# Kernel optimization log

Hardware: AMD Instinct MI355X
Metric: run time of the kernel (lower is better)

## Reference

```python
import jax, jax.numpy as jnp
import numpy as np

VAR0, VAR1 = 0.1, 0.2
THRESHOLD = 0.35
NEGPOS_RATIO = 7
LOW_GT_THRESH = 0.2  # match() filters GT whose best prior IoU < 0.2


def setup_inputs() -> dict:
    key = jax.random.key(0)
    ks = jax.random.split(key, 8)
    B, P, G = 16, 43008, 128
    loc_data = jax.random.normal(ks[0], (B, P, 4), jnp.float32)
    conf_data = jax.random.normal(ks[1], (B, P, 2), jnp.float32)
    landm_data = jax.random.normal(ks[2], (B, P, 10), jnp.float32)
    # priors in cxcywh form, positive sizes
    pc = jax.random.uniform(ks[3], (P, 2), jnp.float32)
    pwh = jax.random.uniform(ks[4], (P, 2), jnp.float32, minval=0.02, maxval=0.32)
    priors = jnp.concatenate([pc, pwh], axis=1)
    # targets: valid xyxy boxes + 10 landmark coords + label (face=1)
    ctr = jax.random.uniform(ks[5], (B, G, 2), jnp.float32, minval=0.2, maxval=0.8)
    wh = jax.random.uniform(ks[6], (B, G, 2), jnp.float32, minval=0.05, maxval=0.3)
    boxes = jnp.concatenate([ctr - wh / 2, ctr + wh / 2], axis=-1)
    landms = jax.random.uniform(ks[7], (B, G, 10), jnp.float32)
    labels = jnp.ones((B, G, 1), jnp.float32)
    targets = jnp.concatenate([boxes, landms, labels], axis=-1)
    return {"loc_data": loc_data, "conf_data": conf_data, "landm_data": landm_data,
            "priors": priors, "targets": targets}


def point_form(priors):
    return jnp.concatenate([priors[:, :2] - priors[:, 2:] / 2,
                            priors[:, :2] + priors[:, 2:] / 2], axis=1)


def jaccard(a, b):  # a: [G,4] xyxy, b: [P,4] xyxy -> [G,P]
    lt = jnp.maximum(a[:, None, :2], b[None, :, :2])
    rb = jnp.minimum(a[:, None, 2:], b[None, :, 2:])
    wh = jnp.clip(rb - lt, 0.0)
    inter = wh[..., 0] * wh[..., 1]
    area_a = (a[:, 2] - a[:, 0]) * (a[:, 3] - a[:, 1])
    area_b = (b[:, 2] - b[:, 0]) * (b[:, 3] - b[:, 1])
    return inter / (area_a[:, None] + area_b[None, :] - inter)


def encode(matched, priors):  # matched xyxy [P,4], priors cxcywh [P,4]
    g_cxcy = (matched[:, :2] + matched[:, 2:]) / 2 - priors[:, :2]
    g_cxcy = g_cxcy / (VAR0 * priors[:, 2:])
    g_wh = jnp.log((matched[:, 2:] - matched[:, :2]) / priors[:, 2:]) / VAR1
    return jnp.concatenate([g_cxcy, g_wh], axis=1)


def encode_landm(matched, priors):  # matched [P,10], priors [P,4]
    m = matched.reshape(-1, 5, 2)
    g = (m - priors[:, None, :2]) / (VAR0 * priors[:, None, 2:])
    return g.reshape(-1, 10)


def match_one(truths, labels, landms, priors):
    G = truths.shape[0]
    overlaps = jaccard(truths, point_form(priors))  # [G, P]
    best_prior_overlap = overlaps.max(axis=1)       # [G]
    best_prior_idx = overlaps.argmax(axis=1)        # [G]
    valid = best_prior_overlap >= LOW_GT_THRESH
    any_valid = jnp.any(valid)
    best_truth_overlap = overlaps.max(axis=0)       # [P]
    best_truth_idx = overlaps.argmax(axis=0)        # [P]
    # index_fill_(0, best_prior_idx_filter, 2): ensure each valid GT keeps its best prior
    fill_val = jnp.where(valid, 2.0, best_truth_overlap[best_prior_idx])
    best_truth_overlap = best_truth_overlap.at[best_prior_idx].set(fill_val)
    # best_truth_idx[best_prior_idx[j]] = j for all j
    best_truth_idx = best_truth_idx.at[best_prior_idx].set(jnp.arange(G))
    matches = truths[best_truth_idx]                       # [P,4]
    conf = labels[best_truth_idx].astype(jnp.int32)        # [P]
    conf = jnp.where(best_truth_overlap < THRESHOLD, 0, conf)
    conf = jnp.where(any_valid, conf, 0)  # no valid GT -> all background
    loc = encode(matches, priors)
    landm = encode_landm(landms[best_truth_idx], priors)
    return loc, conf, landm


def smooth_l1(x):
    ax = jnp.abs(x)
    return jnp.where(ax < 1.0, 0.5 * ax * ax, ax - 0.5)


def reference(loc_data, conf_data, landm_data, priors, targets):
    truths = targets[..., :4]
    landms = targets[..., 4:14]
    labels = targets[..., 14]
    loc_t, conf_t, landm_t = jax.vmap(
        lambda t, l, lm: match_one(t, l, lm, priors))(truths, labels, landms)

    # landmark loss over positives
    pos1 = conf_t > 0
    N1 = jnp.maximum(pos1.sum().astype(jnp.float32), 1.0)
    loss_landm = jnp.sum(smooth_l1(landm_data - landm_t) * pos1[..., None])

    # localization loss over positives
    pos = conf_t != 0
    num_pos = pos.sum(axis=1, keepdims=True)  # [B,1]
    loss_l = jnp.sum(smooth_l1(loc_data - loc_t) * pos[..., None])

    # hard negative mining on per-prior CE loss
    lse = jax.scipy.special.logsumexp(conf_data, axis=-1)  # [B,P]
    gathered = jnp.take_along_axis(conf_data, conf_t[..., None], axis=-1)[..., 0]
    ce_all = lse - gathered                                # [B,P] per-prior CE
    mine = jnp.where(pos, 0.0, ce_all)
    loss_idx = jnp.argsort(-mine, axis=1)
    idx_rank = jnp.argsort(loss_idx, axis=1)
    num_neg = jnp.clip(NEGPOS_RATIO * num_pos, None, pos.shape[1] - 1)
    neg = idx_rank < num_neg
    sel = pos | neg
    loss_c = jnp.sum(jnp.where(sel, ce_all, 0.0))

    N = jnp.maximum(num_pos.sum().astype(jnp.float32), 1.0)
    return loss_l / N, loss_c / N, loss_landm / N1
```

## Files before the change

kernel.cpp:

```cpp
#include <hip/hip_runtime.h>
#include <stdint.h>


#define GC 8
#define PPI 3

__device__ __forceinline__ float sl1(float x) {
  float a = fabsf(x);
  return a < 1.f ? 0.5f * a * a : a - 0.5f;
}

__device__ __forceinline__ double dwave(double v) {
#pragma unroll
  for (int o = 32; o; o >>= 1) v += __shfl_down(v, o);
  return v;
}

__global__ __launch_bounds__(256) void k_match(
    const float* __restrict__ priors, const float* __restrict__ targets,
    float* __restrict__ bto, int* __restrict__ bti,
    unsigned long long* __restrict__ bp, int P, int G, int NIOU, int PT3,
    int NGC, int PC) {
  int tid = threadIdx.x;
  __shared__ float4 sgt[128];
  __shared__ float sga[128];
  __shared__ unsigned long long sred[GC * 256];

  if ((int)blockIdx.x < NIOU) {
    int b = blockIdx.x / PT3, tile = blockIdx.x % PT3;
    int base = tile * (256 * PPI);
    for (int g = tid; g < G; g += 256) {
      const float* t = targets + ((size_t)b * G + g) * 15;
      float x1 = t[0], y1 = t[1], x2 = t[2], y2 = t[3];
      sgt[g] = make_float4(x1, y1, x2, y2);
      sga[g] = (x2 - x1) * (y2 - y1);
    }
    __syncthreads();

    float px1[PPI], py1[PPI], px2[PPI], py2[PPI], pa[PPI];
    float bi[PPI], sb[PPI];
    int bidx[PPI];
#pragma unroll
    for (int k = 0; k < PPI; ++k) {
      int p = base + tid + k * 256;
      int pl = p < P ? p : P - 1;
      float4 pr = ((const float4*)priors)[pl];
      px1[k] = pr.x - pr.z * 0.5f; py1[k] = pr.y - pr.w * 0.5f;
      px2[k] = pr.x + pr.z * 0.5f; py2[k] = pr.y + pr.w * 0.5f;
      pa[k] = pr.z * pr.w;
      bi[k] = 0.f; sb[k] = 1.f; bidx[k] = 0;
    }

    for (int g = 0; g < G; g += 2) {
      float4 T0 = sgt[g];
      float4 T1 = sgt[g + 1];
      float A0 = sga[g];
      float A1 = sga[g + 1];
#pragma unroll
      for (int k = 0; k < PPI; ++k) {
        {
          float iw = fminf(T0.z, px2[k]) - fmaxf(T0.x, px1[k]);
          float ih = fminf(T0.w, py2[k]) - fmaxf(T0.y, py1[k]);
          float inter = fmaxf(iw, 0.f) * fmaxf(ih, 0.f);
          float S = A0 + pa[k];
          if (inter * sb[k] > bi[k] * S) { bi[k] = inter; sb[k] = S; bidx[k] = g; }
        }
        {
          float iw = fminf(T1.z, px2[k]) - fmaxf(T1.x, px1[k]);
          float ih = fminf(T1.w, py2[k]) - fmaxf(T1.y, py1[k]);
          float inter = fmaxf(iw, 0.f) * fmaxf(ih, 0.f);
          float S = A1 + pa[k];
          if (inter * sb[k] > bi[k] * S) { bi[k] = inter; sb[k] = S; bidx[k] = g + 1; }
        }
      }
    }
#pragma unroll
    for (int k = 0; k < PPI; ++k) {
      int p = base + tid + k * 256;
      if (p < P) {
        bto[(size_t)b * P + p] = bi[k] / (sb[k] - bi[k]);
        bti[(size_t)b * P + p] = bidx[k];
      }
    }
  } else {
    int bc = blockIdx.x - NIOU;
    int pc = bc % PC;
    int gcb = (bc / PC) % NGC;
    int b = bc / (PC * NGC);
    int g0 = gcb * GC;

    if (tid < GC) {
      int g = g0 + tid;
      float4 v = make_float4(0.f, 0.f, 0.f, 0.f);
      if (g < G) {
        const float* t = targets + ((size_t)b * G + g) * 15;
        v = make_float4(t[0], t[1], t[2], t[3]);
      }
      sgt[tid] = v;
    }
    __syncthreads();

    float gx1[GC], gy1[GC], gx2[GC], gy2[GC], ga[GC];
#pragma unroll
    for (int j = 0; j < GC; ++j) {
      float4 T = sgt[j];
      gx1[j] = T.x; gy1[j] = T.y; gx2[j] = T.z; gy2[j] = T.w;
      ga[j] = (T.z - T.x) * (T.w - T.y);
    }

    int chunk = (P + PC - 1) / PC;
    int ps = pc * chunk;
    int pe = ps + chunk; if (pe > P) pe = P;
    int count = pe - ps;

    float bi[GC], sb[GC];
    unsigned bpp[GC];
#pragma unroll
    for (int j = 0; j < GC; ++j) { bi[j] = 0.f; sb[j] = 1.f; bpp[j] = (unsigned)(ps + tid); }

    for (int i = tid; i < count; i += 512) {
      int p0 = ps + i;
      int i1 = i + 256;
      int p1 = (i1 < count) ? ps + i1 : p0;
      float4 q0 = ((const float4*)priors)[p0];
      float4 q1 = ((const float4*)priors)[p1];
      float ax1 = q0.x - q0.z * 0.5f, ay1 = q0.y - q0.w * 0.5f;
      float ax2 = q0.x + q0.z * 0.5f, ay2 = q0.y + q0.w * 0.5f;
      float aa = q0.z * q0.w;
      float bx1 = q1.x - q1.z * 0.5f, by1 = q1.y - q1.w * 0.5f;
      float bx2 = q1.x + q1.z * 0.5f, by2 = q1.y + q1.w * 0.5f;
      float ba = q1.z * q1.w;
#pragma unroll
      for (int j = 0; j < GC; ++j) {
        {
          float iw = fminf(gx2[j], ax2) - fmaxf(gx1[j], ax1);
          float ih = fminf(gy2[j], ay2) - fmaxf(gy1[j], ay1);
          float inter = fmaxf(iw, 0.f) * fmaxf(ih, 0.f);
          float S = ga[j] + aa;
          if (inter * sb[j] > bi[j] * S) { bi[j] = inter; sb[j] = S; bpp[j] = (unsigned)p0; }
        }
        {
          float iw = fminf(gx2[j], bx2) - fmaxf(gx1[j], bx1);
          float ih = fminf(gy2[j], by2) - fmaxf(gy1[j], by1);
          float inter = fmaxf(iw, 0.f) * fmaxf(ih, 0.f);
          float S = ga[j] + ba;
          if (inter * sb[j] > bi[j] * S) { bi[j] = inter; sb[j] = S; bpp[j] = (unsigned)p1; }
        }
      }
    }

#pragma unroll
    for (int j = 0; j < GC; ++j) {
      float iou = bi[j] / (sb[j] - bi[j]);
      unsigned long long pk =
          ((unsigned long long)__float_as_uint(iou) << 32) | (unsigned)(~bpp[j]);
      sred[j * 256 + tid] = pk;
    }
    __syncthreads();
    {
      int j = tid >> 5, s = tid & 31;
      unsigned long long m = sred[j * 256 + s];
#pragma unroll
      for (int t = 1; t < 8; ++t) {
        unsigned long long v = sred[j * 256 + s + t * 32];
        if (v > m) m = v;
      }
      __syncthreads();
      sred[j * 256 + s] = m;
    }
    __syncthreads();
    if (tid < GC) {
      unsigned long long m = sred[tid * 256];
      for (int s = 1; s < 32; ++s) {
        unsigned long long v = sred[tid * 256 + s];
        if (v > m) m = v;
      }
      int g = g0 + tid;
      if (g < G) atomicMax(&bp[(size_t)b * G + g], m);
    }
  }
}

__global__ void k_scatter(const unsigned long long* __restrict__ bp,
                          float* __restrict__ bto, int* __restrict__ bti,
                          int* __restrict__ anyv, int P, int G) {
  int b = blockIdx.x, g = threadIdx.x;
  __shared__ unsigned spp[128];
  __shared__ int s_any;
  if (g == 0) s_any = 0;
  __syncthreads();
  unsigned long long m = bp[(size_t)b * G + g];
  unsigned pp = ~(unsigned)m;
  float val = __uint_as_float((unsigned)(m >> 32));
  bool ok = (m != 0ULL);
  float oldv = 0.f;
  if (ok) oldv = bto[(size_t)b * P + pp];
  spp[g] = ok ? pp : 0xFFFFFFFFu;
  if (ok && val >= 0.2f) s_any = 1;
  __syncthreads();
  bool win = ok;
  for (int g2 = g + 1; g2 < G; ++g2)
    if (spp[g2] == pp) win = false;
  if (win) {
    bto[(size_t)b * P + pp] = (val >= 0.2f) ? 2.0f : oldv;
    bti[(size_t)b * P + pp] = g;
  }
  __syncthreads();
  if (g == 0) anyv[b] = s_any;
}

__global__ __launch_bounds__(256) void k_main(
    const float* __restrict__ loc, const float* __restrict__ conf,
    const float* __restrict__ lm, const float* __restrict__ priors,
    const float* __restrict__ targets, const float* __restrict__ bto,
    const int* __restrict__ bti, const int* __restrict__ anyv,
    float* __restrict__ mine, unsigned* __restrict__ h1,
    double* __restrict__ pll, double* __restrict__ pllm,
    double* __restrict__ plc, double* __restrict__ msum,
    int* __restrict__ pnp, int P, int G, int PT) {
  int b = blockIdx.x / PT, tile = blockIdx.x % PT;
  int tid = threadIdx.x;
  int p = tile * 256 + tid;

  __shared__ float st[128 * 15];
  __shared__ unsigned hist[1024];
  __shared__ double rs[16];
  __shared__ int ri[4];

  for (int i = tid; i < G * 15; i += 256) st[i] = targets[(size_t)b * G * 15 + i];
  for (int i = tid; i < 1024; i += 256) hist[i] = 0;
  __syncthreads();

  double ll = 0, llm = 0, lc = 0, ms = 0;
  int np = 0;
  if (p < P) {
    size_t idx = (size_t)b * P + p;
    int av = anyv[b];
    float ov = bto[idx];
    int ti = bti[idx];
    bool pos = av && (ov >= 0.35f);

    float2 c = ((const float2*)conf)[idx];
    float mx = fmaxf(c.x, c.y);
    float lse = mx + logf(expf(c.x - mx) + expf(c.y - mx));
    float ce = lse - (pos ? c.y : c.x);
    float mv = pos ? 0.f : ce;
    mine[idx] = mv;
    ms = (double)mv;
    atomicAdd(&hist[__float_as_uint(mv) >> 21], 1u);

    if (pos) {
      np = 1;
      lc = (double)ce;
      float4 pr = ((const float4*)priors)[p];
      const float* t = st + ti * 15;
      float dx = 0.1f * pr.z, dy = 0.1f * pr.w;
      float gx = ((t[0] + t[2]) * 0.5f - pr.x) / dx;
      float gy = ((t[1] + t[3]) * 0.5f - pr.y) / dy;
      float gw = logf((t[2] - t[0]) / pr.z) * 5.0f;
      float gh = logf((t[3] - t[1]) / pr.w) * 5.0f;
      float4 ld = ((const float4*)loc)[idx];
      ll = (double)(sl1(ld.x - gx) + sl1(ld.y - gy) + sl1(ld.z - gw) +
                    sl1(ld.w - gh));
      const float2* lmd = (const float2*)lm + idx * 5;
      float s = 0.f;
#pragma unroll
      for (int j = 0; j < 5; ++j) {
        float2 lv = lmd[j];
        float ex = (t[4 + 2 * j] - pr.x) / dx;
        float ey = (t[5 + 2 * j] - pr.y) / dy;
        s += sl1(lv.x - ex) + sl1(lv.y - ey);
      }
      llm = (double)s;
    }
  }

  ll = dwave(ll);
  llm = dwave(llm);
  lc = dwave(lc);
  ms = dwave(ms);
#pragma unroll
  for (int o = 32; o; o >>= 1) np += __shfl_down(np, o);
  int lane = tid & 63, wid = tid >> 6;
  if (lane == 0) {
    rs[wid] = ll; rs[4 + wid] = llm; rs[8 + wid] = lc; rs[12 + wid] = ms;
    ri[wid] = np;
  }
  __syncthreads();
  if (tid == 0) {
    pll[blockIdx.x] = rs[0] + rs[1] + rs[2] + rs[3];
    pllm[blockIdx.x] = rs[4] + rs[5] + rs[6] + rs[7];
    plc[blockIdx.x] = rs[8] + rs[9] + rs[10] + rs[11];
    msum[blockIdx.x] = rs[12] + rs[13] + rs[14] + rs[15];
    pnp[blockIdx.x] = ri[0] + ri[1] + ri[2] + ri[3];
  }
  for (int i = tid; i < 1024; i += 256)
    if (hist[i]) atomicAdd(&h1[(size_t)b * 1024 + i], hist[i]);
}

__global__ __launch_bounds__(256) void k_sel1(
    const unsigned* __restrict__ h1, const int* __restrict__ pnp,
    const double* __restrict__ msum, int* __restrict__ num_pos,
    double* __restrict__ msum_b, int P, int PT, int* __restrict__ pfx1,
    int* __restrict__ k1) {
  int b = blockIdx.x, tid = threadIdx.x;
  __shared__ int sn[256];
  __shared__ double sm[256];
  int n = 0;
  double m = 0;
  for (int i = tid; i < PT; i += 256) { n += pnp[b * PT + i]; m += msum[b * PT + i]; }
  sn[tid] = n; sm[tid] = m;
  __syncthreads();
  for (int off = 128; off; off >>= 1) {
    if (tid < off) { sn[tid] += sn[tid + off]; sm[tid] += sm[tid + off]; }
    __syncthreads();
  }
  int npos = sn[0];
  if (tid == 0) { num_pos[b] = npos; msum_b[b] = sm[0]; }

  long long k = 7LL * (long long)npos;
  long long cap = P - 1;
  if (k <= 0) {
    if (tid == 0) { pfx1[b] = -1; k1[b] = 0; }
    return;
  }
  if (k >= cap) {
    if (tid == 0) { pfx1[b] = -2; k1[b] = 0; }
    return;
  }

  const unsigned* h = h1 + (size_t)b * 1024;
  __shared__ unsigned S[256];
  unsigned p0 = h[tid * 4], p1 = h[tid * 4 + 1], p2 = h[tid * 4 + 2],
           p3 = h[tid * 4 + 3];
  S[tid] = p0 + p1 + p2 + p3;
  __syncthreads();
  for (int off = 1; off < 256; off <<= 1) {
    unsigned add = (tid + off < 256) ? S[tid + off] : 0;
    __syncthreads();
    S[tid] += add;
    __syncthreads();
  }
  int cnt = __syncthreads_count((long long)S[tid] >= k);
  if (cnt == 0) {
    if (tid == 0) { pfx1[b] = -1; k1[b] = 0; }
    return;
  }
  int seg = cnt - 1;
  if (tid == seg) {
    long long cum = (seg + 1 < 256) ? (long long)S[seg + 1] : 0;
    unsigned hv[4] = {p0, p1, p2, p3};
    int bin = seg * 4;
    for (int j = 3; j >= 0; --j) {
      if (cum + hv[j] >= k) { bin = seg * 4 + j; break; }
      cum += hv[j];
    }
    pfx1[b] = bin;
    k1[b] = (int)(k - cum);
  }
}

__global__ __launch_bounds__(256) void k_select(
    const float* __restrict__ mine, const int* __restrict__ pfx1,
    const int* __restrict__ k1, double* __restrict__ pfs_b, int P) {
  int b = blockIdx.x, tid = threadIdx.x;
  int pf = pfx1[b];
  if (pf < 0) return;
  const float* mrow = mine + (size_t)b * P;

  __shared__ unsigned hs[2048];
  __shared__ unsigned S[256];
  __shared__ int spf21, sk2;
  __shared__ unsigned stb;
  __shared__ double stie;
  __shared__ double rs[4];

  for (int i = tid; i < 2048; i += 256) hs[i] = 0;
  __syncthreads();
  for (int i = tid; i < P; i += 256) {
    unsigned bits = __float_as_uint(mrow[i]);
    if ((int)(bits >> 21) == pf) atomicAdd(&hs[(bits >> 10) & 2047], 1u);
  }
  __syncthreads();
  {
    unsigned hv[8];
    unsigned s = 0;
#pragma unroll
    for (int j = 0; j < 8; ++j) { hv[j] = hs[tid * 8 + j]; s += hv[j]; }
    S[tid] = s;
    __syncthreads();
    for (int off = 1; off < 256; off <<= 1) {
      unsigned add = (tid + off < 256) ? S[tid + off] : 0;
      __syncthreads();
      S[tid] += add;
      __syncthreads();
    }
    long long k = (long long)k1[b];
    int cnt = __syncthreads_count((long long)S[tid] >= k);
    int seg = cnt - 1;
    if (tid == seg) {
      long long cum = (seg + 1 < 256) ? (long long)S[seg + 1] : 0;
      int bin = seg * 8;
      for (int j = 7; j >= 0; --j) {
        if (cum + hv[j] >= k) { bin = seg * 8 + j; break; }
        cum += hv[j];
      }
      spf21 = (pf << 11) | bin;
      sk2 = (int)(k - cum);
    }
  }
  __syncthreads();
  int pf21 = spf21;

  for (int i = tid; i < 1024; i += 256) hs[i] = 0;
  __syncthreads();
  for (int i = tid; i < P; i += 256) {
    unsigned bits = __float_as_uint(mrow[i]);
    if ((int)(bits >> 10) == pf21) atomicAdd(&hs[bits & 1023], 1u);
  }
  __syncthreads();
  {
    unsigned p0 = hs[tid * 4], p1 = hs[tid * 4 + 1], p2 = hs[tid * 4 + 2],
             p3 = hs[tid * 4 + 3];
    S[tid] = p0 + p1 + p2 + p3;
    __syncthreads();
    for (int off = 1; off < 256; off <<= 1) {
      unsigned add = (tid + off < 256) ? S[tid + off] : 0;
      __syncthreads();
      S[tid] += add;
      __syncthreads();
    }
    long long k = (long long)sk2;
    int cnt = __syncthreads_count((long long)S[tid] >= k);
    int seg = cnt - 1;
    if (tid == seg) {
      long long cum = (seg + 1 < 256) ? (long long)S[seg + 1] : 0;
      unsigned hv[4] = {p0, p1, p2, p3};
      int bin = seg * 4;
      for (int j = 3; j >= 0; --j) {
        if (cum + hv[j] >= k) { bin = seg * 4 + j; break; }
        cum += hv[j];
      }
      unsigned tb = ((unsigned)pf21 << 10) | (unsigned)bin;
      stb = tb;
      stie = (double)(k - cum) * (double)__uint_as_float(tb);
    }
  }
  __syncthreads();

  unsigned tb = stb;
  double v = 0.0;
  for (int i = tid; i < P; i += 256) {
    unsigned bits = __float_as_uint(mrow[i]);
    if (bits > tb) v += (double)__uint_as_float(bits);
  }
  v = dwave(v);
  int lane = tid & 63, wid = tid >> 6;
  if (lane == 0) rs[wid] = v;
  __syncthreads();
  if (tid == 0) pfs_b[b] = rs[0] + rs[1] + rs[2] + rs[3] + stie;
}

__global__ __launch_bounds__(256) void k_fin(
    const double* __restrict__ pll, const double* __restrict__ pllm,
    const double* __restrict__ plc, const double* __restrict__ pfs_b,
    const double* __restrict__ msum_b, const int* __restrict__ num_pos,
    const int* __restrict__ pfx1, float* __restrict__ out, int NBm, int B) {
  int tid = threadIdx.x;
  double a = 0, c = 0, d = 0, f = 0, n = 0;
  for (int i = tid; i < NBm; i += 256) { a += pll[i]; c += pllm[i]; d += plc[i]; }
  for (int i = tid; i < B; i += 256) {
    f += (pfx1[i] == -2) ? msum_b[i] : pfs_b[i];
    n += (double)num_pos[i];
  }
  a = dwave(a); c = dwave(c); d = dwave(d); f = dwave(f); n = dwave(n);
  __shared__ double rs[5 * 4];
  int lane = tid & 63, wid = tid >> 6;
  if (lane == 0) {
    rs[wid] = a; rs[4 + wid] = c; rs[8 + wid] = d;
    rs[12 + wid] = f; rs[16 + wid] = n;
  }
  __syncthreads();
  if (tid == 0) {
    double A = rs[0] + rs[1] + rs[2] + rs[3];
    double C = rs[4] + rs[5] + rs[6] + rs[7];
    double D = rs[8] + rs[9] + rs[10] + rs[11];
    double F = rs[12] + rs[13] + rs[14] + rs[15];
    double N = rs[16] + rs[17] + rs[18] + rs[19];
    if (N < 1.0) N = 1.0;
    out[0] = (float)(A / N);
    out[1] = (float)((D + F) / N);
    out[2] = (float)(C / N);
  }
}

extern "C" void kernel_launch(void* const* d_in, const int* in_sizes, int n_in,
                              void* d_out, int out_size, void* d_ws,
                              size_t ws_size, hipStream_t stream) {
  const float* loc = (const float*)d_in[0];
  const float* conf = (const float*)d_in[1];
  const float* lm = (const float*)d_in[2];
  const float* priors = (const float*)d_in[3];
  const float* targets = (const float*)d_in[4];

  int P = in_sizes[3] / 4;
  int B = in_sizes[0] / (4 * P);
  int G = in_sizes[4] / (15 * B);
  int PT = (P + 255) / 256;
  int PT3 = (P + 256 * PPI - 1) / (256 * PPI);
  int NBm = B * PT;
  int NGC = (G + GC - 1) / GC;
  int PC = 8;
  int NIOU = B * PT3;
  int NBP = B * NGC * PC;

  char* w = (char*)d_ws;
  size_t off = 0;
  unsigned long long* bp = (unsigned long long*)(w + off);
  off += (size_t)B * G * 8;
  double* pfs_b = (double*)(w + off);
  off += (size_t)B * 8;
  int* ctrl = (int*)(w + off);
  off += (size_t)(8 * B) * 4;
  int* anyv = ctrl;
  int* num_pos = ctrl + B;
  int* pfx1 = ctrl + 2 * B;
  int* k1 = ctrl + 3 * B;
  unsigned* h1 = (unsigned*)(w + off);
  off += (size_t)B * 1024 * 4;
  size_t clear_bytes = off;
  off = (off + 255) & ~(size_t)255;
  float* bto = (float*)(w + off);
  off += (size_t)B * P * 4;
  int* bti = (int*)(w + off);
  off += (size_t)B * P * 4;
  float* mine = (float*)(w + off);
  off += (size_t)B * P * 4;
  double* pll = (double*)(w + off);
  off += (size_t)NBm * 8;
  double* pllm = (double*)(w + off);
  off += (size_t)NBm * 8;
  double* plc = (double*)(w + off);
  off += (size_t)NBm * 8;
  double* msum = (double*)(w + off);
  off += (size_t)NBm * 8;
  double* msum_b = (double*)(w + off);
  off += (size_t)B * 8;
  int* pnp = (int*)(w + off);
  off += (size_t)NBm * 4;

  hipMemsetAsync(d_ws, 0, clear_bytes, stream);

  k_match<<<NIOU + NBP, 256, 0, stream>>>(priors, targets, bto, bti, bp, P, G,
                                          NIOU, PT3, NGC, PC);
  k_scatter<<<B, G, 0, stream>>>(bp, bto, bti, anyv, P, G);
  k_main<<<B * PT, 256, 0, stream>>>(loc, conf, lm, priors, targets, bto, bti,
                                     anyv, mine, h1, pll, pllm, plc, msum, pnp,
                                     P, G, PT);
  k_sel1<<<B, 256, 0, stream>>>(h1, pnp, msum, num_pos, msum_b, P, PT, pfx1,
                                k1);
  k_select<<<B, 256, 0, stream>>>(mine, pfx1, k1, pfs_b, P);
  k_fin<<<1, 256, 0, stream>>>(pll, pllm, plc, pfs_b, msum_b, num_pos, pfx1,
                               (float*)d_out, NBm, B);
}
```

Before: 182.4 us.

## Fold scatter into main kernel, merge selection kernels, and widen match tile

Drops the separate scatter kernel. Each main-kernel block now loads the per-GT best-prior words and applies the forced matches for its own tile in shared memory, with the valid-GT flag computed locally. The two selection kernels become one tail kernel, and the full-sum fallback is written directly into the per-batch result. Priors per thread in the IoU match kernel go from 3 to 4. The aim is to cut launches and global round trips; in exchange every main block repeats an O(G^2) duplicate scan.

```diff
diff --git a/kernel.cpp b/kernel.cpp
--- a/kernel.cpp
+++ b/kernel.cpp
@@ -3,7 +3,7 @@
 
 
 #define GC 8
-#define PPI 3
+#define PPI 4
 
 __device__ __forceinline__ float sl1(float x) {
   float a = fabsf(x);
@@ -19,7 +19,7 @@
 __global__ __launch_bounds__(256) void k_match(
     const float* __restrict__ priors, const float* __restrict__ targets,
     float* __restrict__ bto, int* __restrict__ bti,
-    unsigned long long* __restrict__ bp, int P, int G, int NIOU, int PT3,
+    unsigned long long* __restrict__ bp, int P, int G, int NIOU, int PTI,
     int NGC, int PC) {
   int tid = threadIdx.x;
   __shared__ float4 sgt[128];
@@ -27,7 +27,7 @@
   __shared__ unsigned long long sred[GC * 256];
 
   if ((int)blockIdx.x < NIOU) {
-    int b = blockIdx.x / PT3, tile = blockIdx.x % PT3;
+    int b = blockIdx.x / PTI, tile = blockIdx.x % PTI;
     int base = tile * (256 * PPI);
     for (int g = tid; g < G; g += 256) {
       const float* t = targets + ((size_t)b * G + g) * 15;
@@ -181,63 +181,61 @@
   }
 }
 
-__global__ void k_scatter(const unsigned long long* __restrict__ bp,
-                          float* __restrict__ bto, int* __restrict__ bti,
-                          int* __restrict__ anyv, int P, int G) {
-  int b = blockIdx.x, g = threadIdx.x;
-  __shared__ unsigned spp[128];
-  __shared__ int s_any;
-  if (g == 0) s_any = 0;
-  __syncthreads();
-  unsigned long long m = bp[(size_t)b * G + g];
-  unsigned pp = ~(unsigned)m;
-  float val = __uint_as_float((unsigned)(m >> 32));
-  bool ok = (m != 0ULL);
-  float oldv = 0.f;
-  if (ok) oldv = bto[(size_t)b * P + pp];
-  spp[g] = ok ? pp : 0xFFFFFFFFu;
-  if (ok && val >= 0.2f) s_any = 1;
-  __syncthreads();
-  bool win = ok;
-  for (int g2 = g + 1; g2 < G; ++g2)
-    if (spp[g2] == pp) win = false;
-  if (win) {
-    bto[(size_t)b * P + pp] = (val >= 0.2f) ? 2.0f : oldv;
-    bti[(size_t)b * P + pp] = g;
-  }
-  __syncthreads();
-  if (g == 0) anyv[b] = s_any;
-}
-
 __global__ __launch_bounds__(256) void k_main(
     const float* __restrict__ loc, const float* __restrict__ conf,
     const float* __restrict__ lm, const float* __restrict__ priors,
     const float* __restrict__ targets, const float* __restrict__ bto,
-    const int* __restrict__ bti, const int* __restrict__ anyv,
+    const int* __restrict__ bti, const unsigned long long* __restrict__ bp,
     float* __restrict__ mine, unsigned* __restrict__ h1,
     double* __restrict__ pll, double* __restrict__ pllm,
     double* __restrict__ plc, double* __restrict__ msum,
     int* __restrict__ pnp, int P, int G, int PT) {
   int b = blockIdx.x / PT, tile = blockIdx.x % PT;
   int tid = threadIdx.x;
-  int p = tile * 256 + tid;
+  int base = tile * 256;
+  int p = base + tid;
 
   __shared__ float st[128 * 15];
   __shared__ unsigned hist[1024];
+  __shared__ unsigned long long sbp[128];
+  __shared__ short forced[256];
+  __shared__ int s_any;
   __shared__ double rs[16];
   __shared__ int ri[4];
 
   for (int i = tid; i < G * 15; i += 256) st[i] = targets[(size_t)b * G * 15 + i];
   for (int i = tid; i < 1024; i += 256) hist[i] = 0;
+  if (tid < G) sbp[tid] = bp[(size_t)b * G + tid];
+  forced[tid] = -1;
+  if (tid == 0) s_any = 0;
+  __syncthreads();
+
+  if (tid < G) {
+    unsigned long long m = sbp[tid];
+    unsigned pp = ~(unsigned)m;
+    float val = __uint_as_float((unsigned)(m >> 32));
+    if (val >= 0.2f) s_any = 1;
+    bool win = true;
+    for (int g2 = tid + 1; g2 < G; ++g2)
+      if ((~(unsigned)sbp[g2]) == pp) { win = false; break; }
+    int local = (int)pp - base;
+    if (win && local >= 0 && local < 256)
+      forced[local] = (short)((tid << 1) | (val >= 0.2f ? 1 : 0));
+  }
   __syncthreads();
 
   double ll = 0, llm = 0, lc = 0, ms = 0;
   int np = 0;
   if (p < P) {
     size_t idx = (size_t)b * P + p;
-    int av = anyv[b];
+    int av = s_any;
     float ov = bto[idx];
     int ti = bti[idx];
+    int f = forced[tid];
+    if (f >= 0) {
+      ti = f >> 1;
+      if (f & 1) ov = 2.0f;
+    }
     bool pos = av && (ov >= 0.35f);
 
     float2 c = ((const float2*)conf)[idx];
@@ -298,14 +296,20 @@
     if (hist[i]) atomicAdd(&h1[(size_t)b * 1024 + i], hist[i]);
 }
 
-__global__ __launch_bounds__(256) void k_sel1(
+__global__ __launch_bounds__(256) void k_tail(
     const unsigned* __restrict__ h1, const int* __restrict__ pnp,
-    const double* __restrict__ msum, int* __restrict__ num_pos,
-    double* __restrict__ msum_b, int P, int PT, int* __restrict__ pfx1,
-    int* __restrict__ k1) {
+    const double* __restrict__ msum, const float* __restrict__ mine,
+    int* __restrict__ num_pos, double* __restrict__ pfs_b, int P, int PT) {
   int b = blockIdx.x, tid = threadIdx.x;
   __shared__ int sn[256];
   __shared__ double sm[256];
+  __shared__ unsigned hs[2048];
+  __shared__ unsigned S[256];
+  __shared__ int spf1, sk1, spf21, sk2;
+  __shared__ unsigned stb;
+  __shared__ double stie;
+  __shared__ double rs[4];
+
   int n = 0;
   double m = 0;
   for (int i = tid; i < PT; i += 256) { n += pnp[b * PT + i]; m += msum[b * PT + i]; }
@@ -316,78 +320,21 @@
     __syncthreads();
   }
   int npos = sn[0];
-  if (tid == 0) { num_pos[b] = npos; msum_b[b] = sm[0]; }
+  if (tid == 0) num_pos[b] = npos;
 
   long long k = 7LL * (long long)npos;
   long long cap = P - 1;
-  if (k <= 0) {
-    if (tid == 0) { pfx1[b] = -1; k1[b] = 0; }
+  if (k <= 0) return;
+  if (k >= cap) {
+    if (tid == 0) pfs_b[b] = sm[0];
     return;
   }
-  if (k >= cap) {
-    if (tid == 0) { pfx1[b] = -2; k1[b] = 0; }
-    return;
-  }
-
-  const unsigned* h = h1 + (size_t)b * 1024;
-  __shared__ unsigned S[256];
-  unsigned p0 = h[tid * 4], p1 = h[tid * 4 + 1], p2 = h[tid * 4 + 2],
-           p3 = h[tid * 4 + 3];
-  S[tid] = p0 + p1 + p2 + p3;
-  __syncthreads();
-  for (int off = 1; off < 256; off <<= 1) {
-    unsigned add = (tid + off < 256) ? S[tid + off] : 0;
-    __syncthreads();
-    S[tid] += add;
-    __syncthreads();
-  }
-  int cnt = __syncthreads_count((long long)S[tid] >= k);
-  if (cnt == 0) {
-    if (tid == 0) { pfx1[b] = -1; k1[b] = 0; }
-    return;
-  }
-  int seg = cnt - 1;
-  if (tid == seg) {
-    long long cum = (seg + 1 < 256) ? (long long)S[seg + 1] : 0;
-    unsigned hv[4] = {p0, p1, p2, p3};
-    int bin = seg * 4;
-    for (int j = 3; j >= 0; --j) {
-      if (cum + hv[j] >= k) { bin = seg * 4 + j; break; }
-      cum += hv[j];
-    }
-    pfx1[b] = bin;
-    k1[b] = (int)(k - cum);
-  }
-}
-
-__global__ __launch_bounds__(256) void k_select(
-    const float* __restrict__ mine, const int* __restrict__ pfx1,
-    const int* __restrict__ k1, double* __restrict__ pfs_b, int P) {
-  int b = blockIdx.x, tid = threadIdx.x;
-  int pf = pfx1[b];
-  if (pf < 0) return;
-  const float* mrow = mine + (size_t)b * P;
-
-  __shared__ unsigned hs[2048];
-  __shared__ unsigned S[256];
-  __shared__ int spf21, sk2;
-  __shared__ unsigned stb;
-  __shared__ double stie;
-  __shared__ double rs[4];
-
-  for (int i = tid; i < 2048; i += 256) hs[i] = 0;
-  __syncthreads();
-  for (int i = tid; i < P; i += 256) {
-    unsigned bits = __float_as_uint(mrow[i]);
-    if ((int)(bits >> 21) == pf) atomicAdd(&hs[(bits >> 10) & 2047], 1u);
-  }
-  __syncthreads();
+
   {
-    unsigned hv[8];
-    unsigned s = 0;
-#pragma unroll
-    for (int j = 0; j < 8; ++j) { hv[j] = hs[tid * 8 + j]; s += hv[j]; }
-    S[tid] = s;
+    const unsigned* h = h1 + (size_t)b * 1024;
+    unsigned p0 = h[tid * 4], p1 = h[tid * 4 + 1], p2 = h[tid * 4 + 2],
+             p3 = h[tid * 4 + 3];
+    S[tid] = p0 + p1 + p2 + p3;
     __syncthreads();
     for (int off = 1; off < 256; off <<= 1) {
       unsigned add = (tid + off < 256) ? S[tid + off] : 0;
@@ -395,42 +342,6 @@
       S[tid] += add;
       __syncthreads();
     }
-    long long k = (long long)k1[b];
-    int cnt = __syncthreads_count((long long)S[tid] >= k);
-    int seg = cnt - 1;
-    if (tid == seg) {
-      long long cum = (seg + 1 < 256) ? (long long)S[seg + 1] : 0;
-      int bin = seg * 8;
-      for (int j = 7; j >= 0; --j) {
-        if (cum + hv[j] >= k) { bin = seg * 8 + j; break; }
-        cum += hv[j];
-      }
-      spf21 = (pf << 11) | bin;
-      sk2 = (int)(k - cum);
-    }
-  }
-  __syncthreads();
-  int pf21 = spf21;
-
-  for (int i = tid; i < 1024; i += 256) hs[i] = 0;
-  __syncthreads();
-  for (int i = tid; i < P; i += 256) {
-    unsigned bits = __float_as_uint(mrow[i]);
-    if ((int)(bits >> 10) == pf21) atomicAdd(&hs[bits & 1023], 1u);
-  }
-  __syncthreads();
-  {
-    unsigned p0 = hs[tid * 4], p1 = hs[tid * 4 + 1], p2 = hs[tid * 4 + 2],
-             p3 = hs[tid * 4 + 3];
-    S[tid] = p0 + p1 + p2 + p3;
-    __syncthreads();
-    for (int off = 1; off < 256; off <<= 1) {
-      unsigned add = (tid + off < 256) ? S[tid + off] : 0;
-      __syncthreads();
-      S[tid] += add;
-      __syncthreads();
-    }
-    long long k = (long long)sk2;
     int cnt = __syncthreads_count((long long)S[tid] >= k);
     int seg = cnt - 1;
     if (tid == seg) {
@@ -441,9 +352,83 @@
         if (cum + hv[j] >= k) { bin = seg * 4 + j; break; }
         cum += hv[j];
       }
+      spf1 = bin;
+      sk1 = (int)(k - cum);
+    }
+  }
+  __syncthreads();
+  int pf = spf1;
+  const float* mrow = mine + (size_t)b * P;
+
+  for (int i = tid; i < 2048; i += 256) hs[i] = 0;
+  __syncthreads();
+  for (int i = tid; i < P; i += 256) {
+    unsigned bits = __float_as_uint(mrow[i]);
+    if ((int)(bits >> 21) == pf) atomicAdd(&hs[(bits >> 10) & 2047], 1u);
+  }
+  __syncthreads();
+  {
+    unsigned hv[8];
+    unsigned s = 0;
+#pragma unroll
+    for (int j = 0; j < 8; ++j) { hv[j] = hs[tid * 8 + j]; s += hv[j]; }
+    S[tid] = s;
+    __syncthreads();
+    for (int off = 1; off < 256; off <<= 1) {
+      unsigned add = (tid + off < 256) ? S[tid + off] : 0;
+      __syncthreads();
+      S[tid] += add;
+      __syncthreads();
+    }
+    long long kk = (long long)sk1;
+    int cnt = __syncthreads_count((long long)S[tid] >= kk);
+    int seg = cnt - 1;
+    if (tid == seg) {
+      long long cum = (seg + 1 < 256) ? (long long)S[seg + 1] : 0;
+      int bin = seg * 8;
+      for (int j = 7; j >= 0; --j) {
+        if (cum + hv[j] >= kk) { bin = seg * 8 + j; break; }
+        cum += hv[j];
+      }
+      spf21 = (pf << 11) | bin;
+      sk2 = (int)(kk - cum);
+    }
+  }
+  __syncthreads();
+  int pf21 = spf21;
+
+  for (int i = tid; i < 1024; i += 256) hs[i] = 0;
+  __syncthreads();
+  for (int i = tid; i < P; i += 256) {
+    unsigned bits = __float_as_uint(mrow[i]);
+    if ((int)(bits >> 10) == pf21) atomicAdd(&hs[bits & 1023], 1u);
+  }
+  __syncthreads();
+  {
+    unsigned p0 = hs[tid * 4], p1 = hs[tid * 4 + 1], p2 = hs[tid * 4 + 2],
+             p3 = hs[tid * 4 + 3];
+    S[tid] = p0 + p1 + p2 + p3;
+    __syncthreads();
+    for (int off = 1; off < 256; off <<= 1) {
+      unsigned add = (tid + off < 256) ? S[tid + off] : 0;
+      __syncthreads();
+      S[tid] += add;
+      __syncthreads();
+    }
+    long long kk = (long long)sk2;
+    int cnt = __syncthreads_count((long long)S[tid] >= kk);
+    int seg = cnt - 1;
+    if (tid == seg) {
+      long long cum = (seg + 1 < 256) ? (long long)S[seg + 1] : 0;
+      unsigned hv[4] = {p0, p1, p2, p3};
+      int bin = seg * 4;
+      for (int j = 3; j >= 0; --j) {
+        if (cum + hv[j] >= kk) { bin = seg * 4 + j; break; }
+        cum += hv[j];
+      }
       unsigned tb = ((unsigned)pf21 << 10) | (unsigned)bin;
       stb = tb;
-      stie = (double)(k - cum) * (double)__uint_as_float(tb);
+      stie = (double)(kk - cum) * (double)__uint_as_float(tb);
     }
   }
   __syncthreads();
@@ -464,15 +449,11 @@
 __global__ __launch_bounds__(256) void k_fin(
     const double* __restrict__ pll, const double* __restrict__ pllm,
     const double* __restrict__ plc, const double* __restrict__ pfs_b,
-    const double* __restrict__ msum_b, const int* __restrict__ num_pos,
-    const int* __restrict__ pfx1, float* __restrict__ out, int NBm, int B) {
+    const int* __restrict__ num_pos, float* __restrict__ out, int NBm, int B) {
   int tid = threadIdx.x;
   double a = 0, c = 0, d = 0, f = 0, n = 0;
   for (int i = tid; i < NBm; i += 256) { a += pll[i]; c += pllm[i]; d += plc[i]; }
-  for (int i = tid; i < B; i += 256) {
-    f += (pfx1[i] == -2) ? msum_b[i] : pfs_b[i];
-    n += (double)num_pos[i];
-  }
+  for (int i = tid; i < B; i += 256) { f += pfs_b[i]; n += (double)num_pos[i]; }
   a = dwave(a); c = dwave(c); d = dwave(d); f = dwave(f); n = dwave(n);
   __shared__ double rs[5 * 4];
   int lane = tid & 63, wid = tid >> 6;
@@ -507,11 +488,11 @@
   int B = in_sizes[0] / (4 * P);
   int G = in_sizes[4] / (15 * B);
   int PT = (P + 255) / 256;
-  int PT3 = (P + 256 * PPI - 1) / (256 * PPI);
+  int PTI = (P + 256 * PPI - 1) / (256 * PPI);
   int NBm = B * PT;
   int NGC = (G + GC - 1) / GC;
   int PC = 8;
-  int NIOU = B * PT3;
+  int NIOU = B * PTI;
   int NBP = B * NGC * PC;
 
   char* w = (char*)d_ws;
@@ -520,12 +501,9 @@
   off += (size_t)B * G * 8;
   double* pfs_b = (double*)(w + off);
   off += (size_t)B * 8;
-  int* ctrl = (int*)(w + off);
-  off += (size_t)(8 * B) * 4;
-  int* anyv = ctrl;
-  int* num_pos = ctrl + B;
-  int* pfx1 = ctrl + 2 * B;
-  int* k1 = ctrl + 3 * B;
+  int* num_pos = (int*)(w + off);
+  off += (size_t)B * 4;
+  off = (off + 7) & ~(size_t)7;
   unsigned* h1 = (unsigned*)(w + off);
   off += (size_t)B * 1024 * 4;
   size_t clear_bytes = off;
@@ -544,22 +522,17 @@
   off += (size_t)NBm * 8;
   double* msum = (double*)(w + off);
   off += (size_t)NBm * 8;
-  double* msum_b = (double*)(w + off);
-  off += (size_t)B * 8;
   int* pnp = (int*)(w + off);
   off += (size_t)NBm * 4;
 
   hipMemsetAsync(d_ws, 0, clear_bytes, stream);
 
   k_match<<<NIOU + NBP, 256, 0, stream>>>(priors, targets, bto, bti, bp, P, G,
-                                          NIOU, PT3, NGC, PC);
-  k_scatter<<<B, G, 0, stream>>>(bp, bto, bti, anyv, P, G);
+                                          NIOU, PTI, NGC, PC);
   k_main<<<B * PT, 256, 0, stream>>>(loc, conf, lm, priors, targets, bto, bti,
-                                     anyv, mine, h1, pll, pllm, plc, msum, pnp,
+                                     bp, mine, h1, pll, pllm, plc, msum, pnp,
                                      P, G, PT);
-  k_sel1<<<B, 256, 0, stream>>>(h1, pnp, msum, num_pos, msum_b, P, PT, pfx1,
-                                k1);
-  k_select<<<B, 256, 0, stream>>>(mine, pfx1, k1, pfs_b, P);
-  k_fin<<<1, 256, 0, stream>>>(pll, pllm, plc, pfs_b, msum_b, num_pos, pfx1,
-                               (float*)d_out, NBm, B);
-}
+  k_tail<<<B, 256, 0, stream>>>(h1, pnp, msum, mine, num_pos, pfs_b, P, PT);
+  k_fin<<<1, 256, 0, stream>>>(pll, pllm, plc, pfs_b, num_pos, (float*)d_out,
+                               NBm, B);
+}
```

New measurement: 196.3 us. 1.08x slower.
